# Performance work log

Hardware: AMD Instinct MI355X
Metric: run time of the kernel (lower is better)

## Reference

```python
import jax, jax.numpy as jnp
import numpy as np

# dims
B, FIN, FOUT = 4, 64, 32
FMID = min(FIN, FOUT)          # fmiddle
NCLS, NH = 4, 64               # num_classes, SPADE nhidden
S = 32                         # D = H = W
EPS = 1e-5


def conv3d(x, w, b=None, pad=1):
    # x: [N,C,D,H,W], w: [O,I,kd,kh,kw]
    out = jax.lax.conv_general_dilated(
        x, w, window_strides=(1, 1, 1), padding=[(pad, pad)] * 3,
        dimension_numbers=('NCDHW', 'OIDHW', 'NCDHW'))
    if b is not None:
        out = out + b[None, :, None, None, None]
    return out


def instance_norm(x):
    # per-sample, per-channel over spatial dims (InstanceNorm3d, affine=False)
    mu = x.mean(axis=(2, 3, 4), keepdims=True)
    var = x.var(axis=(2, 3, 4), keepdims=True)
    return (x - mu) * jax.lax.rsqrt(var + EPS)


def spade(x, y, Ws, Bs, Wg, Bg, Wb, Bb):
    # x: [B,C,D,H,W]; param stacks have leading num_classes dim; y routes per sample.
    normalized = instance_norm(x)
    ws, bs, wg, bg, wb, bb = Ws[y], Bs[y], Wg[y], Bg[y], Wb[y], Bb[y]

    def one(xi, wsi, bsi, wgi, bgi, wbi, bbi):
        xi = xi[None]  # [1,C,D,H,W]
        actv = jax.nn.relu(conv3d(xi, wsi, bsi))
        gamma = conv3d(actv, wgi, bgi)[0]
        beta = conv3d(actv, wbi, bbi)[0]
        return gamma, beta

    gamma, beta = jax.vmap(one)(x, ws, bs, wg, bg, wb, bb)
    return normalized * (1.0 + gamma) + beta


def _lrelu(t):
    return jax.nn.leaky_relu(t, 0.2)


def setup_inputs() -> dict:
    key = jax.random.key(0)
    ks = jax.random.split(key, 24)
    sc = 0.05
    inp = {
        'x': jax.random.normal(ks[0], (B, FIN, S, S, S), jnp.float32),
        'y': jax.random.randint(ks[1], (B,), 0, NCLS, jnp.int64
                                if jax.config.jax_enable_x64 else jnp.int32),
        # SPADE norm_0 stacks: label_nc = norm_nc = FIN
        's0_ws': jax.random.normal(ks[2], (NCLS, NH, FIN, 3, 3, 3), jnp.float32) * sc,
        's0_bs': jnp.zeros((NCLS, NH), jnp.float32),
        's0_wg': jax.random.normal(ks[3], (NCLS, FIN, NH, 3, 3, 3), jnp.float32) * sc,
        's0_bg': jnp.zeros((NCLS, FIN), jnp.float32),
        's0_wb': jax.random.normal(ks[4], (NCLS, FIN, NH, 3, 3, 3), jnp.float32) * sc,
        's0_bb': jnp.zeros((NCLS, FIN), jnp.float32),
        # SPADE norm_1 stacks: label_nc = norm_nc = FMID
        's1_ws': jax.random.normal(ks[5], (NCLS, NH, FMID, 3, 3, 3), jnp.float32) * sc,
        's1_bs': jnp.zeros((NCLS, NH), jnp.float32),
        's1_wg': jax.random.normal(ks[6], (NCLS, FMID, NH, 3, 3, 3), jnp.float32) * sc,
        's1_bg': jnp.zeros((NCLS, FMID), jnp.float32),
        's1_wb': jax.random.normal(ks[7], (NCLS, FMID, NH, 3, 3, 3), jnp.float32) * sc,
        's1_bb': jnp.zeros((NCLS, FMID), jnp.float32),
        # resnet convs
        'conv0_w': jax.random.normal(ks[8], (FMID, FIN, 3, 3, 3), jnp.float32) * sc,
        'conv0_b': jnp.zeros((FMID,), jnp.float32),
        'conv1_w': jax.random.normal(ks[9], (FOUT, FMID, 3, 3, 3), jnp.float32) * sc,
        'conv1_b': jnp.zeros((FOUT,), jnp.float32),
        'convs_w': jax.random.normal(ks[10], (FOUT, FIN, 1, 1, 1), jnp.float32) * sc,
    }
    return inp


def reference(x, y, s0_ws, s0_bs, s0_wg, s0_bg, s0_wb, s0_bb,
              s1_ws, s1_bs, s1_wg, s1_bg, s1_wb, s1_bb,
              conv0_w, conv0_b, conv1_w, conv1_b, convs_w):
    x_s = conv3d(x, convs_w, None, pad=0)  # learned shortcut (fin != fout, no bias)
    dx = conv3d(_lrelu(spade(x, y, s0_ws, s0_bs, s0_wg, s0_bg, s0_wb, s0_bb)),
                conv0_w, conv0_b)
    dx = conv3d(_lrelu(spade(dx, y, s1_ws, s1_bs, s1_wg, s1_bg, s1_wb, s1_bb)),
                conv1_w, conv1_b)
    return x_s + dx
```

## Files before the change

### kernel.cpp

```cpp
#include <hip/hip_runtime.h>


#define S3 32768
constexpr float EPS = 1e-5f;

typedef __attribute__((ext_vector_type(8))) short s16x8;
typedef __attribute__((ext_vector_type(4))) float f32x4;
typedef __attribute__((ext_vector_type(16))) float f32x16;
typedef __attribute__((ext_vector_type(4))) unsigned short u16x4;
typedef __attribute__((ext_vector_type(8))) unsigned short u16x8;

#define GLL(g, l)                                                        \
  __builtin_amdgcn_global_load_lds(                                      \
      (const __attribute__((address_space(1))) void*)(g),                \
      (__attribute__((address_space(3))) void*)(l), 16, 0, 0)

__device__ __forceinline__ float bf2f(unsigned short u) {
  union { unsigned int i; float f; } v; v.i = ((unsigned int)u) << 16; return v.f;
}
__device__ __forceinline__ unsigned short f2bf(float f) {
  union { float f; unsigned int i; } v; v.f = f;
  unsigned int r = (v.i + 0x7FFFu + ((v.i >> 16) & 1u)) >> 16;
  return (unsigned short)r;
}

__global__ __launch_bounds__(256) void stats_kernel(const float* __restrict__ x,
                                                    float* __restrict__ mu,
                                                    float* __restrict__ rstd) {
  const int bc = blockIdx.x;
  const float* p = x + (size_t)bc * S3;
  float s = 0.f, s2 = 0.f;
  for (int i = threadIdx.x; i < S3 / 4; i += 256) {
    float4 v = reinterpret_cast<const float4*>(p)[i];
    s  += v.x + v.y + v.z + v.w;
    s2 += v.x * v.x + v.y * v.y + v.z * v.z + v.w * v.w;
  }
  for (int off = 32; off; off >>= 1) {
    s  += __shfl_down(s, off, 64);
    s2 += __shfl_down(s2, off, 64);
  }
  __shared__ float ls[4], ls2[4];
  const int wid = threadIdx.x >> 6;
  if ((threadIdx.x & 63) == 0) { ls[wid] = s; ls2[wid] = s2; }
  __syncthreads();
  if (threadIdx.x == 0) {
    float S = 0.f, S2 = 0.f;
    for (int i = 0; i < 4; ++i) { S += ls[i]; S2 += ls2[i]; }
    const float m = S / (float)S3;
    const float var = S2 / (float)S3 - m * m;
    mu[bc] = m;
    rstd[bc] = rsqrtf(var + EPS);
  }
}

__global__ __launch_bounds__(256) void stats_t32_p1(const short* __restrict__ t,
                                                    float* __restrict__ part) {
  const int b = blockIdx.y;
  const int chunk = blockIdx.x;
  const int tid = threadIdx.x;
  const int pq = tid & 3;
  float s[8], s2[8];
#pragma unroll
  for (int j = 0; j < 8; ++j) { s[j] = 0.f; s2[j] = 0.f; }
  const int vbase = chunk * 512;
#pragma unroll
  for (int v = tid >> 2; v < 512; v += 64) {
    u16x8 u = *reinterpret_cast<const u16x8*>(
        &t[((size_t)b * S3 + vbase + v) * 32 + pq * 8]);
#pragma unroll
    for (int j = 0; j < 8; ++j) { float f = bf2f(u[j]); s[j] += f; s2[j] += f * f; }
  }
#pragma unroll
  for (int off = 4; off < 64; off <<= 1) {
#pragma unroll
    for (int j = 0; j < 8; ++j) {
      s[j]  += __shfl_xor(s[j], off, 64);
      s2[j] += __shfl_xor(s2[j], off, 64);
    }
  }
  __shared__ float red[4][4][16];
  const int wv = tid >> 6, lane = tid & 63;
  if (lane < 4) {
#pragma unroll
    for (int j = 0; j < 8; ++j) { red[wv][lane][j] = s[j]; red[wv][lane][8 + j] = s2[j]; }
  }
  __syncthreads();
  if (tid < 32) {
    const int p = tid >> 3, j = tid & 7;
    float S = 0.f, S2 = 0.f;
#pragma unroll
    for (int w = 0; w < 4; ++w) { S += red[w][p][j]; S2 += red[w][p][8 + j]; }
    const int c = p * 8 + j;
    part[((size_t)(b * 64 + chunk)) * 64 + c] = S;
    part[((size_t)(b * 64 + chunk)) * 64 + 32 + c] = S2;
  }
}

__global__ __launch_bounds__(128) void stats_t32_p2(const float* __restrict__ part,
                                                    float* __restrict__ mu,
                                                    float* __restrict__ rstd) {
  const int tid = threadIdx.x;
  const int b = tid >> 5, c = tid & 31;
  float S = 0.f, S2 = 0.f;
#pragma unroll 4
  for (int k = 0; k < 64; ++k) {
    S  += part[((size_t)(b * 64 + k)) * 64 + c];
    S2 += part[((size_t)(b * 64 + k)) * 64 + 32 + c];
  }
  const float m = S / (float)S3;
  const float var = S2 / (float)S3 - m * m;
  mu[b * 32 + c] = m;
  rstd[b * 32 + c] = rsqrtf(var + EPS);
}

__global__ __launch_bounds__(256) void transpose_x(const float* __restrict__ x,
                                                   short* __restrict__ xt) {
  const int b = blockIdx.y;
  const int v0 = blockIdx.x * 64;
  __shared__ unsigned short t[64][72];
  const int vox = threadIdx.x & 63;
  const int cg = threadIdx.x >> 6;
#pragma unroll
  for (int k = 0; k < 16; ++k) {
    const int ci = cg * 16 + k;
    t[vox][ci] = f2bf(x[((size_t)(b * 64 + ci)) * S3 + v0 + vox]);
  }
  __syncthreads();
  const int vv = threadIdx.x >> 2, part = threadIdx.x & 3;
  uint4 u0 = *reinterpret_cast<const uint4*>(&t[vv][part * 16]);
  uint4 u1 = *reinterpret_cast<const uint4*>(&t[vv][part * 16 + 8]);
  short* dst = &xt[((size_t)(b * S3 + v0 + vv)) * 64 + part * 16];
  *reinterpret_cast<uint4*>(dst) = u0;
  *reinterpret_cast<uint4*>(dst + 8) = u1;
}

__global__ __launch_bounds__(256) void repack_w(
    const float* __restrict__ wA, const float* __restrict__ wB,
    short* __restrict__ dst, const int* __restrict__ y,
    int CBLK, int CO2, int CI, long clsA, long clsB, int paired, int total) {
  const int b = blockIdx.y;
  const int idx = blockIdx.x * 256 + threadIdx.x;
  if (idx >= total) return;
  const int cls = y[b];
  const int KCH = CI / 16;
  const int ci = idx & 15;
  const int co = (idx >> 4) % CO2;
  const int rest = idx / (16 * CO2);
  const int k16 = rest % KCH;
  const int tap = rest / KCH;
  const int srcch = k16 * 16 + ci;
  float v;
  if (paired) {
    const int H = CBLK >> 1;
    const int blk = co / CBLK, w = co % CBLK;
    if (w < H)
      v = wA[(size_t)clsA * cls + ((size_t)(blk * H + w) * CI + srcch) * 27 + tap];
    else
      v = wB[(size_t)clsB * cls + ((size_t)(blk * H + w - H) * CI + srcch) * 27 + tap];
  } else {
    v = wA[(size_t)clsA * cls + ((size_t)co * CI + srcch) * 27 + tap];
  }
  dst[(((size_t)(b * 27 + tap) * KCH + k16) * CO2 + co) * 16 + ci] = (short)f2bf(v);
}

template <int CIN, int CBLK, int COTOT, int EPI, int NNORM>
__global__ __launch_bounds__(256, 2) void conv_mfma(
    const short* __restrict__ xt,
    const short* __restrict__ W,
    const float* __restrict__ bias,
    int bias_stride,
    const int* __restrict__ y,
    const short* __restrict__ xnb,
    const float* __restrict__ mu,
    const float* __restrict__ rstd,
    const float* __restrict__ bgs,
    const float* __restrict__ bbs,
    const short* __restrict__ zp,
    float* __restrict__ outf,
    short* __restrict__ outb) {
  constexpr int KCH = CIN / 16;
  constexpr int NCOG = CBLK / 32;
  constexpr int PG = 604;
  constexpr int XG = 2 * PG;

  __shared__ short ldsX[2][XG * 8];

  const int tid = threadIdx.x;
  const int lane = tid & 63, wid = tid >> 6;
  const int l31 = lane & 31, khf = lane >> 5;
  const int b = blockIdx.y;
  const int cls = y[b];
  const int co_base = blockIdx.z * CBLK;
  const int tile = blockIdx.x;
  const int d0 = (tile >> 4) * 4, h0 = ((tile >> 2) & 3) * 8, w0 = (tile & 3) * 8;

  const short* gsrc[5];
#pragma unroll
  for (int k = 0; k < 5; ++k) {
    const int i = tid + k * 256;
    const short* g = zp;
    if (i < XG) {
      const int pl = (i >= PG) ? 1 : 0;
      const int slot = i - pl * PG;
      if (slot < 600) {
        const int sd = slot / 100, r0 = slot - sd * 100;
        const int sh = r0 / 10, sw0 = r0 - sh * 10;
        const int gd = d0 + sd - 1, gh = h0 + sh - 1, gw = w0 + sw0 - 1;
        if ((unsigned)gd < 32u && (unsigned)gh < 32u && (unsigned)gw < 32u)
          g = xt + ((size_t)b * S3 + gd * 1024 + gh * 32 + gw) * CIN + pl * 8;
      }
    }
    gsrc[k] = g;
  }

  auto stage_x = [&](int kc, int xbuf) {
#pragma unroll
    for (int k = 0; k < 5; ++k) {
      const int i = tid + k * 256;
      if (i < XG) GLL(gsrc[k] + kc * 16, &ldsX[xbuf][i * 8]);
    }
  };

  f32x16 acc[2][NCOG];
#pragma unroll
  for (int v = 0; v < 2; ++v)
#pragma unroll
    for (int c = 0; c < NCOG; ++c)
#pragma unroll
      for (int r = 0; r < 16; ++r) acc[v][c][r] = 0.f;

  const int hw10 = (l31 >> 3) * 10 + (l31 & 7);
  const int xpl = khf * PG;
  const int wlane = (co_base + l31) * 16 + khf * 8;

  stage_x(0, 0);
  __syncthreads();

  int xb = 0;
#pragma unroll
  for (int kc = 0; kc < KCH; ++kc) {
#pragma unroll
    for (int kd = 0; kd < 3; ++kd) {
      s16x8 af[9][NCOG];
#pragma unroll
      for (int t9 = 0; t9 < 9; ++t9)
#pragma unroll
        for (int c = 0; c < NCOG; ++c)
          af[t9][c] = *reinterpret_cast<const s16x8*>(
              &W[(((size_t)(b * 27 + kd * 9 + t9) * KCH + kc) * COTOT) * 16 +
                 wlane + c * 512]);
      if (kd == 0 && kc + 1 < KCH) stage_x(kc + 1, xb ^ 1);

      __builtin_amdgcn_s_setprio(1);
#pragma unroll
      for (int kh = 0; kh < 3; ++kh) {
#pragma unroll
        for (int kw = 0; kw < 3; ++kw) {
          const int t9 = kh * 3 + kw;
          s16x8 bf[2];
#pragma unroll
          for (int vg = 0; vg < 2; ++vg) {
            const int slot = (wid + kd) * 100 + (vg * 4 + kh) * 10 + kw + hw10;
            bf[vg] = *reinterpret_cast<const s16x8*>(&ldsX[xb][(xpl + slot) * 8]);
          }
#pragma unroll
          for (int c = 0; c < NCOG; ++c)
#pragma unroll
            for (int vg = 0; vg < 2; ++vg)
              acc[vg][c] = __builtin_amdgcn_mfma_f32_32x32x16_bf16(
                  af[t9][c], bf[vg], acc[vg][c], 0, 0, 0);
        }
      }
      __builtin_amdgcn_s_setprio(0);
    }
    __syncthreads();
    xb ^= 1;
  }

  const int dgv = (d0 + wid) * 1024 + (h0 + (l31 >> 3)) * 32 + w0 + (l31 & 7);

  if constexpr (EPI == 0 || EPI == 1) {
#pragma unroll
    for (int c = 0; c < NCOG; ++c)
#pragma unroll
      for (int q = 0; q < 4; ++q) {
        const int c0 = co_base + c * 32 + q * 8 + khf * 4;
        const f32x4 b4 = *reinterpret_cast<const f32x4*>(&bias[cls * bias_stride + c0]);
#pragma unroll
        for (int vg = 0; vg < 2; ++vg) {
          const int gv = dgv + vg * 128;
          u16x4 o;
#pragma unroll
          for (int rr = 0; rr < 4; ++rr) {
            float v = acc[vg][c][q * 4 + rr] + b4[rr];
            if constexpr (EPI == 0) v = fmaxf(v, 0.f);
            o[rr] = f2bf(v);
          }
          *reinterpret_cast<u16x4*>(&outb[((size_t)b * S3 + gv) * COTOT + c0]) = o;
        }
      }
  }

  if constexpr (EPI == 2) {
    const int nb = blockIdx.z * 32;
#pragma unroll
    for (int q = 0; q < 4; ++q) {
      const int c0 = nb + q * 8 + khf * 4;
      const f32x4 m4  = *reinterpret_cast<const f32x4*>(&mu[b * NNORM + c0]);
      const f32x4 r4  = *reinterpret_cast<const f32x4*>(&rstd[b * NNORM + c0]);
      const f32x4 g4  = *reinterpret_cast<const f32x4*>(&bgs[cls * NNORM + c0]);
      const f32x4 bb4 = *reinterpret_cast<const f32x4*>(&bbs[cls * NNORM + c0]);
#pragma unroll
      for (int vg = 0; vg < 2; ++vg) {
        const int gv = dgv + vg * 128;
        const size_t vgl = (size_t)b * S3 + gv;
        u16x4 u = *reinterpret_cast<const u16x4*>(&xnb[vgl * NNORM + c0]);
        u16x4 o;
#pragma unroll
        for (int rr = 0; rr < 4; ++rr) {
          const float gamma = acc[vg][0][q * 4 + rr] + g4[rr];
          const float beta  = acc[vg][1][q * 4 + rr] + bb4[rr];
          const float nrm = (bf2f(u[rr]) - m4[rr]) * r4[rr];
          float h = nrm * (1.f + gamma) + beta;
          h = h > 0.f ? h : 0.2f * h;
          o[rr] = f2bf(h);
        }
        *reinterpret_cast<u16x4*>(&outb[vgl * NNORM + c0]) = o;
      }
    }
  }

  if constexpr (EPI == 4) {
#pragma unroll
    for (int q = 0; q < 4; ++q) {
      const int c0 = q * 8 + khf * 4;
      const f32x4 b4 = *reinterpret_cast<const f32x4*>(&bias[c0]);
#pragma unroll
      for (int vg = 0; vg < 2; ++vg) {
        const int gv = dgv + vg * 128;
#pragma unroll
        for (int rr = 0; rr < 4; ++rr) {
          float* p = &outf[((size_t)(b * 32 + c0 + rr)) * S3 + gv];
          *p += acc[vg][0][q * 4 + rr] + b4[rr];
        }
      }
    }
  }
}

__global__ __launch_bounds__(256) void shortcut_kernel(const float* __restrict__ x,
                                                       const float* __restrict__ wsc,
                                                       float* __restrict__ out) {
  const int b = blockIdx.y;
  const int v = blockIdx.x * 256 + threadIdx.x;
  __shared__ float lw[64 * 32];
  for (int i = threadIdx.x; i < 2048; i += 256) {
    int ci = i >> 5, o = i & 31;
    lw[i] = wsc[o * 64 + ci];
  }
  __syncthreads();
  float acc[32];
#pragma unroll
  for (int o = 0; o < 32; ++o) acc[o] = 0.f;
  const float* xp = x + (size_t)b * 64 * S3 + v;
#pragma unroll 1
  for (int ci = 0; ci < 64; ++ci) {
    const float xv = xp[(size_t)ci * S3];
    const float4* wp = reinterpret_cast<const float4*>(&lw[ci << 5]);
#pragma unroll
    for (int o4 = 0; o4 < 8; ++o4) {
      float4 w4 = wp[o4];
      acc[o4 * 4 + 0] += xv * w4.x;
      acc[o4 * 4 + 1] += xv * w4.y;
      acc[o4 * 4 + 2] += xv * w4.z;
      acc[o4 * 4 + 3] += xv * w4.w;
    }
  }
  float* op = out + (size_t)b * 32 * S3 + v;
#pragma unroll
  for (int o = 0; o < 32; ++o) op[(size_t)o * S3] = acc[o];
}

extern "C" void kernel_launch(void* const* d_in, const int* in_sizes, int n_in,
                              void* d_out, int out_size, void* d_ws, size_t ws_size,
                              hipStream_t stream) {
  const float* x       = (const float*)d_in[0];
  const int*   y       = (const int*)d_in[1];
  const float* s0_ws   = (const float*)d_in[2];
  const float* s0_bs   = (const float*)d_in[3];
  const float* s0_wg   = (const float*)d_in[4];
  const float* s0_bg   = (const float*)d_in[5];
  const float* s0_wb   = (const float*)d_in[6];
  const float* s0_bb   = (const float*)d_in[7];
  const float* s1_ws   = (const float*)d_in[8];
  const float* s1_bs   = (const float*)d_in[9];
  const float* s1_wg   = (const float*)d_in[10];
  const float* s1_bg   = (const float*)d_in[11];
  const float* s1_wb   = (const float*)d_in[12];
  const float* s1_bb   = (const float*)d_in[13];
  const float* conv0_w = (const float*)d_in[14];
  const float* conv0_b = (const float*)d_in[15];
  const float* conv1_w = (const float*)d_in[16];
  const float* conv1_b = (const float*)d_in[17];
  const float* convs_w = (const float*)d_in[18];

  float* out = (float*)d_out;
  char* ws = (char*)d_ws;
  short* xt    = (short*)(ws);
  short* actvT = (short*)(ws + 16777216);
  short* hT    = (short*)(ws + 33554432);
  short* d0T   = (short*)(ws + 50331648);
  short* Wa0   = (short*)(ws + 58720256);
  short* Ws0   = (short*)(ws + 60817408);
  short* Wc0   = (short*)(ws + 62914560);
  short* Wa1   = (short*)(ws + 65011712);
  short* Ws1   = (short*)(ws + 67108864);
  short* Wc1   = (short*)(ws + 69206016);
  short* zp    = (short*)(ws + 70254592);
  float* stats = (float*)(ws + 71303168);
  float* mu0 = stats, *rstd0 = stats + 256, *mu1 = stats + 512, *rstd1 = stats + 640;
  float* spart = stats + 1024;

  hipMemsetAsync(zp, 0, 4096, stream);

  transpose_x<<<dim3(512, 4), 256, 0, stream>>>(x, xt);
  stats_kernel<<<dim3(256), 256, 0, stream>>>(x, mu0, rstd0);

  repack_w<<<dim3(432, 4), 256, 0, stream>>>(s0_ws, nullptr, Wa0, y, 64, 64, 64,
                                             64L * 64 * 27, 0, 0, 110592);
  repack_w<<<dim3(864, 4), 256, 0, stream>>>(s0_wg, s0_wb, Ws0, y, 64, 128, 64,
                                             64L * 64 * 27, 64L * 64 * 27, 1, 221184);
  repack_w<<<dim3(216, 4), 256, 0, stream>>>(conv0_w, nullptr, Wc0, y, 32, 32, 64,
                                             0, 0, 0, 55296);
  repack_w<<<dim3(216, 4), 256, 0, stream>>>(s1_ws, nullptr, Wa1, y, 64, 64, 32,
                                             64L * 32 * 27, 0, 0, 55296);
  repack_w<<<dim3(432, 4), 256, 0, stream>>>(s1_wg, s1_wb, Ws1, y, 64, 64, 64,
                                             32L * 64 * 27, 32L * 64 * 27, 1, 110592);
  repack_w<<<dim3(108, 4), 256, 0, stream>>>(conv1_w, nullptr, Wc1, y, 32, 32, 32,
                                             0, 0, 0, 27648);

  conv_mfma<64, 64, 64, 0, 0><<<dim3(128, 4, 1), 256, 0, stream>>>(
      xt, Wa0, s0_bs, 64, y, nullptr, nullptr, nullptr, nullptr, nullptr, zp,
      nullptr, actvT);
  conv_mfma<64, 64, 128, 2, 64><<<dim3(128, 4, 2), 256, 0, stream>>>(
      actvT, Ws0, nullptr, 0, y, xt, mu0, rstd0, s0_bg, s0_bb, zp,
      nullptr, hT);
  conv_mfma<64, 32, 32, 1, 0><<<dim3(128, 4, 1), 256, 0, stream>>>(
      hT, Wc0, conv0_b, 0, y, nullptr, nullptr, nullptr, nullptr, nullptr, zp,
      nullptr, d0T);
  stats_t32_p1<<<dim3(64, 4), 256, 0, stream>>>(d0T, spart);
  stats_t32_p2<<<dim3(1), 128, 0, stream>>>(spart, mu1, rstd1);
  conv_mfma<32, 64, 64, 0, 0><<<dim3(128, 4, 1), 256, 0, stream>>>(
      d0T, Wa1, s1_bs, 64, y, nullptr, nullptr, nullptr, nullptr, nullptr, zp,
      nullptr, actvT);
  conv_mfma<64, 64, 64, 2, 32><<<dim3(128, 4, 1), 256, 0, stream>>>(
      actvT, Ws1, nullptr, 0, y, d0T, mu1, rstd1, s1_bg, s1_bb, zp,
      nullptr, hT);
  shortcut_kernel<<<dim3(128, 4), 256, 0, stream>>>(x, convs_w, out);
  conv_mfma<32, 32, 32, 4, 0><<<dim3(128, 4, 1), 256, 0, stream>>>(
      hT, Wc1, conv1_b, 0, y, nullptr, nullptr, nullptr, nullptr, nullptr, zp,
      out, nullptr);
}
```

Before: 313.0 us.

## Software-pipeline weight fragment loads across phases with explicit vmcnt waits

Restructures the conv MFMA main loop into a flat sequence of phases, one per (kc, kd) pair. Each weight fragment for the next phase is prefetched right after its MFMAs consume the current one, which hides global weight-load latency behind compute. Input staging moves to the last kd phase and is synchronised with manual vmcnt waits and raw s_barrier instead of __syncthreads. The LDS layout also changes: the per-plane padding is dropped and every lane issues all five global-to-LDS loads unconditionally, with out-of-range lanes loading zeros. This adds dummy loads and relies on vmcnt ordering being correct.

```diff
diff --git a/kernel.cpp b/kernel.cpp
--- a/kernel.cpp
+++ b/kernel.cpp
@@ -14,6 +14,11 @@
   __builtin_amdgcn_global_load_lds(                                      \
       (const __attribute__((address_space(1))) void*)(g),                \
       (__attribute__((address_space(3))) void*)(l), 16, 0, 0)
+
+template <int N>
+__device__ __forceinline__ void wait_vm() {
+  asm volatile("s_waitcnt vmcnt(%0)" ::"n"(N) : "memory");
+}
 
 __device__ __forceinline__ float bf2f(unsigned short u) {
   union { unsigned int i; float f; } v; v.i = ((unsigned int)u) << 16; return v.f;
@@ -179,9 +184,12 @@
     float* __restrict__ outf,
     short* __restrict__ outb) {
   constexpr int KCH = CIN / 16;
+  constexpr int NPH = 3 * KCH;
   constexpr int NCOG = CBLK / 32;
-  constexpr int PG = 604;
-  constexpr int XG = 2 * PG;
+  constexpr int XG = 1280;
+  constexpr int XISS = 5;
+  constexpr long TS  = (long)KCH * COTOT * 16;
+  constexpr long KCS = (long)COTOT * 16;
 
   __shared__ short ldsX[2][XG * 8];
 
@@ -194,88 +202,106 @@
   const int tile = blockIdx.x;
   const int d0 = (tile >> 4) * 4, h0 = ((tile >> 2) & 3) * 8, w0 = (tile & 3) * 8;
 
-  const short* gsrc[5];
-#pragma unroll
-  for (int k = 0; k < 5; ++k) {
+  const short* gsrc[XISS];
+#pragma unroll
+  for (int k = 0; k < XISS; ++k) {
     const int i = tid + k * 256;
     const short* g = zp;
-    if (i < XG) {
-      const int pl = (i >= PG) ? 1 : 0;
-      const int slot = i - pl * PG;
-      if (slot < 600) {
-        const int sd = slot / 100, r0 = slot - sd * 100;
-        const int sh = r0 / 10, sw0 = r0 - sh * 10;
-        const int gd = d0 + sd - 1, gh = h0 + sh - 1, gw = w0 + sw0 - 1;
-        if ((unsigned)gd < 32u && (unsigned)gh < 32u && (unsigned)gw < 32u)
-          g = xt + ((size_t)b * S3 + gd * 1024 + gh * 32 + gw) * CIN + pl * 8;
+    if (i < 1200) {
+      const int pl = (i >= 600) ? 1 : 0;
+      const int slot = i - pl * 600;
+      const int sd = slot / 100, r0 = slot - sd * 100;
+      const int sh = r0 / 10, sw0 = r0 - sh * 10;
+      const int gd = d0 + sd - 1, gh = h0 + sh - 1, gw = w0 + sw0 - 1;
+      if ((unsigned)gd < 32u && (unsigned)gh < 32u && (unsigned)gw < 32u)
+        g = xt + ((size_t)b * S3 + gd * 1024 + gh * 32 + gw) * CIN + pl * 8;
+    }
+    gsrc[k] = g;
+  }
+
+  auto stage_x = [&](int kc, int xbuf) {
+    const bool real = kc < KCH;
+#pragma unroll
+    for (int k = 0; k < XISS; ++k) {
+      const int i = tid + k * 256;
+      GLL(real ? gsrc[k] + kc * 16 : zp, &ldsX[xbuf][i * 8]);
+    }
+  };
+
+  f32x16 acc[2][NCOG];
+#pragma unroll
+  for (int v = 0; v < 2; ++v)
+#pragma unroll
+    for (int c = 0; c < NCOG; ++c)
+#pragma unroll
+      for (int r = 0; r < 16; ++r) acc[v][c][r] = 0.f;
+
+  const int hw10 = (l31 >> 3) * 10 + (l31 & 7);
+  const int xpl = khf * 600;
+
+  const short* WL = W + (size_t)b * 27 * TS + (co_base + l31) * 16 + khf * 8;
+
+  s16x8 af[9][NCOG];
+#pragma unroll
+  for (int t9 = 0; t9 < 9; ++t9)
+#pragma unroll
+    for (int c = 0; c < NCOG; ++c)
+      af[t9][c] = *reinterpret_cast<const s16x8*>(WL + t9 * TS + c * 512);
+  stage_x(0, 0);
+  wait_vm<0>();
+  __builtin_amdgcn_sched_barrier(0);
+  __builtin_amdgcn_s_barrier();
+  __builtin_amdgcn_sched_barrier(0);
+
+  int xb = 0;
+#pragma unroll
+  for (int p = 0; p < NPH; ++p) {
+    const int kc = p / 3, kd = p % 3;
+    if (kd == 2) {
+      stage_x(kc + 1, xb ^ 1);
+      __builtin_amdgcn_sched_barrier(0);
+    }
+    const int np = p + 1;
+    const bool real = np < NPH;
+    const short* nbase = real ? (WL + (np / 3) * KCS + (size_t)(np % 3) * 9 * TS) : zp;
+    const long nts = real ? TS : 0;
+    const int ncs = real ? 512 : 0;
+
+    __builtin_amdgcn_s_setprio(1);
+#pragma unroll
+    for (int kh = 0; kh < 3; ++kh) {
+#pragma unroll
+      for (int kw = 0; kw < 3; ++kw) {
+        const int t9 = kh * 3 + kw;
+        s16x8 bf[2];
+#pragma unroll
+        for (int vg = 0; vg < 2; ++vg) {
+          const int slot = (wid + kd) * 100 + (vg * 4 + kh) * 10 + kw + hw10;
+          bf[vg] = *reinterpret_cast<const s16x8*>(&ldsX[xb][(xpl + slot) * 8]);
+        }
+#pragma unroll
+        for (int c = 0; c < NCOG; ++c)
+#pragma unroll
+          for (int vg = 0; vg < 2; ++vg)
+            acc[vg][c] = __builtin_amdgcn_mfma_f32_32x32x16_bf16(
+                af[t9][c], bf[vg], acc[vg][c], 0, 0, 0);
+#pragma unroll
+        for (int c = 0; c < NCOG; ++c)
+          af[t9][c] = *reinterpret_cast<const s16x8*>(nbase + t9 * nts + c * ncs);
       }
     }
-    gsrc[k] = g;
-  }
-
-  auto stage_x = [&](int kc, int xbuf) {
-#pragma unroll
-    for (int k = 0; k < 5; ++k) {
-      const int i = tid + k * 256;
-      if (i < XG) GLL(gsrc[k] + kc * 16, &ldsX[xbuf][i * 8]);
-    }
-  };
-
-  f32x16 acc[2][NCOG];
-#pragma unroll
-  for (int v = 0; v < 2; ++v)
-#pragma unroll
-    for (int c = 0; c < NCOG; ++c)
-#pragma unroll
-      for (int r = 0; r < 16; ++r) acc[v][c][r] = 0.f;
-
-  const int hw10 = (l31 >> 3) * 10 + (l31 & 7);
-  const int xpl = khf * PG;
-  const int wlane = (co_base + l31) * 16 + khf * 8;
-
-  stage_x(0, 0);
-  __syncthreads();
-
-  int xb = 0;
-#pragma unroll
-  for (int kc = 0; kc < KCH; ++kc) {
-#pragma unroll
-    for (int kd = 0; kd < 3; ++kd) {
-      s16x8 af[9][NCOG];
-#pragma unroll
-      for (int t9 = 0; t9 < 9; ++t9)
-#pragma unroll
-        for (int c = 0; c < NCOG; ++c)
-          af[t9][c] = *reinterpret_cast<const s16x8*>(
-              &W[(((size_t)(b * 27 + kd * 9 + t9) * KCH + kc) * COTOT) * 16 +
-                 wlane + c * 512]);
-      if (kd == 0 && kc + 1 < KCH) stage_x(kc + 1, xb ^ 1);
-
-      __builtin_amdgcn_s_setprio(1);
-#pragma unroll
-      for (int kh = 0; kh < 3; ++kh) {
-#pragma unroll
-        for (int kw = 0; kw < 3; ++kw) {
-          const int t9 = kh * 3 + kw;
-          s16x8 bf[2];
-#pragma unroll
-          for (int vg = 0; vg < 2; ++vg) {
-            const int slot = (wid + kd) * 100 + (vg * 4 + kh) * 10 + kw + hw10;
-            bf[vg] = *reinterpret_cast<const s16x8*>(&ldsX[xb][(xpl + slot) * 8]);
-          }
-#pragma unroll
-          for (int c = 0; c < NCOG; ++c)
-#pragma unroll
-            for (int vg = 0; vg < 2; ++vg)
-              acc[vg][c] = __builtin_amdgcn_mfma_f32_32x32x16_bf16(
-                  af[t9][c], bf[vg], acc[vg][c], 0, 0, 0);
-        }
-      }
-      __builtin_amdgcn_s_setprio(0);
-    }
-    __syncthreads();
-    xb ^= 1;
-  }
+    __builtin_amdgcn_s_setprio(0);
+
+    if (kd == 2) {
+      wait_vm<9 * NCOG>();
+      __builtin_amdgcn_sched_barrier(0);
+      __builtin_amdgcn_s_barrier();
+      __builtin_amdgcn_sched_barrier(0);
+      xb ^= 1;
+    }
+  }
+  wait_vm<0>();
+  __builtin_amdgcn_sched_barrier(0);
 
   const int dgv = (d0 + wid) * 1024 + (h0 + (l31 >> 3)) * 32 + w0 + (l31 & 7);
 
```

Result: slower. 335.7 us (+7.2%).
